# Performance work log

Hardware: AMD Instinct MI355X
Metric: run time of the kernel (lower is better)

Reference implementation:

```python
import jax, jax.numpy as jnp
import numpy as np

N = 100000   # nodes
E = 1600000  # edges (avg degree 16)
N_IN, N_HID, N_OUT = 64, 64, 16


def setup_inputs() -> dict:
    key = jax.random.key(0)
    k1, k2, k3, k4 = jax.random.split(key, 4)
    x = jax.random.normal(k1, (N, N_IN), dtype=jnp.float32)
    edge_index = jax.random.randint(k2, (2, E), 0, N, dtype=jnp.int64)
    # Glorot-style init like PyG GCNConv linear weights
    W1 = jax.random.normal(k3, (N_IN, N_HID), dtype=jnp.float32) * (1.0 / np.sqrt(N_IN))
    b1 = jnp.zeros((N_HID,), dtype=jnp.float32)
    W2 = jax.random.normal(k4, (N_HID, N_OUT), dtype=jnp.float32) * (1.0 / np.sqrt(N_HID))
    b2 = jnp.zeros((N_OUT,), dtype=jnp.float32)
    return {"x": x, "edge_index": edge_index, "W1": W1, "b1": b1, "W2": W2, "b2": b2}


def reference(x, edge_index, W1, b1, W2, b2):
    n = x.shape[0]
    # GCNConv default: add self-loops with weight 1, symmetric normalization
    loop = jnp.arange(n, dtype=edge_index.dtype)
    src = jnp.concatenate([edge_index[0], loop])  # [E+N]
    dst = jnp.concatenate([edge_index[1], loop])  # [E+N]
    w = jnp.ones(src.shape[0], dtype=x.dtype)
    deg = jax.ops.segment_sum(w, dst, num_segments=n)           # in-degree incl. self-loop
    dinv = jnp.where(deg > 0, jax.lax.rsqrt(deg), 0.0)
    norm = dinv[src] * w * dinv[dst]                            # [E+N] edge coefficients

    def gcn_conv(h, Wm, bm):
        h = h @ Wm                                              # [N, d_out] linear first (PyG order)
        msg = h[src] * norm[:, None]                            # gather + scale
        return jax.ops.segment_sum(msg, dst, num_segments=n) + bm  # scatter-add + bias

    h = jax.nn.relu(gcn_conv(x, W1, b1))
    # dropout is identity at inference (training=False)
    return jax.nn.log_softmax(gcn_conv(h, W2, b2), axis=1)
```

## Files before the change

kernel.cpp:

```cpp
#include <hip/hip_runtime.h>

constexpr int FIN = 64;
constexpr int FH  = 64;
constexpr int FO  = 16;


constexpr int BSH   = 7;
constexpr int BW    = 1 << BSH;
constexpr int NBUCK = 1024;
constexpr int EPB   = 16384;

constexpr int XT_STRIDE = 68;

__device__ inline unsigned short f2bf(float f) {
    unsigned u = __float_as_uint(f);
    return (unsigned short)((u + 0x7FFFu + ((u >> 16) & 1u)) >> 16);
}
__device__ inline float bf2f(unsigned short h) {
    return __uint_as_float((unsigned)h << 16);
}
__device__ inline float4 bf4_to_f4(ushort4 u) {
    float4 f;
    f.x = bf2f(u.x); f.y = bf2f(u.y); f.z = bf2f(u.z); f.w = bf2f(u.w);
    return f;
}

__launch_bounds__(256)
__global__ void gemm1_hist_kernel(const float* __restrict__ x, const float* __restrict__ W1,
                                  unsigned short* __restrict__ hsb,
                                  const int* __restrict__ ei, int E,
                                  int* __restrict__ bcnt, int N, int G1T) {
    __shared__ float smem[FIN * FH + 64 * XT_STRIDE];
    int tid = threadIdx.x;
    if ((int)blockIdx.x >= G1T) {
        int* lh = (int*)smem;
        for (int i = tid; i < NBUCK; i += 256) lh[i] = 0;
        __syncthreads();
        int base = ((int)blockIdx.x - G1T) * EPB;
        int lim  = min(E, base + EPB);
        for (int e = base + tid; e < lim; e += 256)
            atomicAdd(&lh[ei[E + e] >> BSH], 1);
        __syncthreads();
        for (int b = tid; b < NBUCK; b += 256) {
            int c = lh[b];
            if (c > 0) atomicAdd(&bcnt[b], c);
        }
        return;
    }
    float* Ws  = smem;
    float* xsT = smem + FIN * FH;
    {
        const float4* W14 = (const float4*)W1;
        float4* Ws4 = (float4*)Ws;
        for (int i = tid; i < 1024; i += 256) Ws4[i] = W14[i];
    }
    int rowBase = blockIdx.x * 64;
    const float4* x4 = (const float4*)x;
    #pragma unroll
    for (int p = 0; p < 4; ++p) {
        int f   = tid + p * 256;
        int row = f >> 4;
        int c4  = f & 15;
        int grow = rowBase + row;
        float4 v = (grow < N) ? x4[(size_t)grow * 16 + c4]
                              : make_float4(0.f, 0.f, 0.f, 0.f);
        xsT[(c4 * 4 + 0) * XT_STRIDE + row] = v.x;
        xsT[(c4 * 4 + 1) * XT_STRIDE + row] = v.y;
        xsT[(c4 * 4 + 2) * XT_STRIDE + row] = v.z;
        xsT[(c4 * 4 + 3) * XT_STRIDE + row] = v.w;
    }
    __syncthreads();
    int cg = tid & 15;
    int rg = tid >> 4;
    float4 a0 = {0,0,0,0}, a1 = {0,0,0,0}, a2 = {0,0,0,0}, a3 = {0,0,0,0};
    #pragma unroll 8
    for (int k = 0; k < FIN; ++k) {
        float4 wv = *(const float4*)&Ws[k * FH + cg * 4];
        float4 xv = *(const float4*)&xsT[k * XT_STRIDE + rg * 4];
        a0.x = fmaf(xv.x, wv.x, a0.x); a0.y = fmaf(xv.x, wv.y, a0.y);
        a0.z = fmaf(xv.x, wv.z, a0.z); a0.w = fmaf(xv.x, wv.w, a0.w);
        a1.x = fmaf(xv.y, wv.x, a1.x); a1.y = fmaf(xv.y, wv.y, a1.y);
        a1.z = fmaf(xv.y, wv.z, a1.z); a1.w = fmaf(xv.y, wv.w, a1.w);
        a2.x = fmaf(xv.z, wv.x, a2.x); a2.y = fmaf(xv.z, wv.y, a2.y);
        a2.z = fmaf(xv.z, wv.z, a2.z); a2.w = fmaf(xv.z, wv.w, a2.w);
        a3.x = fmaf(xv.w, wv.x, a3.x); a3.y = fmaf(xv.w, wv.y, a3.y);
        a3.z = fmaf(xv.w, wv.z, a3.z); a3.w = fmaf(xv.w, wv.w, a3.w);
    }
    ushort4* hsb4 = (ushort4*)hsb;
    {
        int grow = rowBase + rg * 4 + 0;
        if (grow < N) hsb4[(size_t)grow * 16 + cg] =
            make_ushort4(f2bf(a0.x), f2bf(a0.y), f2bf(a0.z), f2bf(a0.w));
        grow = rowBase + rg * 4 + 1;
        if (grow < N) hsb4[(size_t)grow * 16 + cg] =
            make_ushort4(f2bf(a1.x), f2bf(a1.y), f2bf(a1.z), f2bf(a1.w));
        grow = rowBase + rg * 4 + 2;
        if (grow < N) hsb4[(size_t)grow * 16 + cg] =
            make_ushort4(f2bf(a2.x), f2bf(a2.y), f2bf(a2.z), f2bf(a2.w));
        grow = rowBase + rg * 4 + 3;
        if (grow < N) hsb4[(size_t)grow * 16 + cg] =
            make_ushort4(f2bf(a3.x), f2bf(a3.y), f2bf(a3.z), f2bf(a3.w));
    }
}

__launch_bounds__(1024)
__global__ void bucket_scan_kernel(const int* __restrict__ bcnt, int* __restrict__ bbase,
                                   int* __restrict__ gcur, int* __restrict__ offs,
                                   int N, int E) {
    __shared__ int s[NBUCK];
    int t = threadIdx.x;
    int v = bcnt[t];
    s[t] = v;
    __syncthreads();
    for (int d = 1; d < NBUCK; d <<= 1) {
        int u = (t >= d) ? s[t - d] : 0;
        __syncthreads();
        s[t] += u;
        __syncthreads();
    }
    int ex = s[t] - v;
    bbase[t] = ex;
    gcur[t]  = ex;
    if (t == NBUCK - 1) {
        bbase[NBUCK] = s[t];
        offs[N] = E;
    }
}

__launch_bounds__(256)
__global__ void binning_kernel(const int* __restrict__ ei, int E,
                               int* __restrict__ gcur, unsigned* __restrict__ ebuf) {
    __shared__ int lh[NBUCK];
    int t = threadIdx.x;
    for (int i = t; i < NBUCK; i += 256) lh[i] = 0;
    __syncthreads();
    int base = blockIdx.x * EPB;
    int lim  = min(E, base + EPB);
    for (int e = base + t; e < lim; e += 256)
        atomicAdd(&lh[ei[E + e] >> BSH], 1);
    __syncthreads();
    for (int b = t; b < NBUCK; b += 256) {
        int c = lh[b];
        lh[b] = (c > 0) ? atomicAdd(&gcur[b], c) : 0;
    }
    __syncthreads();
    for (int e = base + t; e < lim; e += 256) {
        int d = ei[E + e];
        int srcv = ei[e];
        int pos = atomicAdd(&lh[d >> BSH], 1);
        ebuf[pos] = (unsigned)srcv | ((unsigned)(d & (BW - 1)) << 17);
    }
}

__launch_bounds__(256)
__global__ void bucket_csr_kernel(const unsigned* __restrict__ ebuf,
                                  const int* __restrict__ bbase,
                                  int* __restrict__ csr, int* __restrict__ offs,
                                  float* __restrict__ dinv, int N) {
    __shared__ int cnt[BW], sc[BW], cur[BW];
    int t = threadIdx.x;
    int b = blockIdx.x;
    if (t < BW) cnt[t] = 0;
    __syncthreads();
    int beg = bbase[b], end = bbase[b + 1];
    for (int i = beg + t; i < end; i += 256)
        atomicAdd(&cnt[ebuf[i] >> 17], 1);
    __syncthreads();
    if (t < BW) sc[t] = cnt[t];
    __syncthreads();
    for (int d = 1; d < BW; d <<= 1) {
        int u = (t < BW && t >= d) ? sc[t - d] : 0;
        __syncthreads();
        if (t < BW) sc[t] += u;
        __syncthreads();
    }
    int nodeBase = b << BSH;
    if (t < BW) {
        int node = nodeBase + t;
        int ex = beg + sc[t] - cnt[t];
        cur[t] = ex;
        if (node < N) {
            offs[node] = ex;
            dinv[node] = rsqrtf((float)(cnt[t] + 1));
        }
    }
    __syncthreads();
    for (int i = beg + t; i < end; i += 256) {
        unsigned w = ebuf[i];
        int pos = atomicAdd(&cur[w >> 17], 1);
        csr[pos] = (int)(w & 0x1FFFF);
    }
}

__launch_bounds__(256)
__global__ void agg1_gemm2_kernel(const unsigned short* __restrict__ hsb,
                                  const int* __restrict__ csr,
                                  const int* __restrict__ offs, const float* __restrict__ dinv,
                                  const float* __restrict__ b1, const float* __restrict__ W2,
                                  unsigned short* __restrict__ hs2b, int N) {
    __shared__ float W2s[FH * FO];
    __shared__ float h1s[16][68];
    const ushort4* hs4 = (const ushort4*)hsb;
    int tid = threadIdx.x;
    for (int i = tid; i < FH * FO; i += 256) W2s[i] = W2[i];
    int g = tid >> 4, l = tid & 15;
    int n = blockIdx.x * 16 + g;
    if (n < N) {
        float di_n = dinv[n];
        float4 self = bf4_to_f4(hs4[(size_t)n * 16 + l]);
        float4 acc;
        acc.x = self.x * di_n; acc.y = self.y * di_n;
        acc.z = self.z * di_n; acc.w = self.w * di_n;
        int j = offs[n], end = offs[n + 1];
        for (; j + 1 < end; j += 2) {
            int s0 = csr[j], s1 = csr[j + 1];
            float d0 = dinv[s0], d1 = dinv[s1];
            float4 a = bf4_to_f4(hs4[(size_t)s0 * 16 + l]);
            float4 b = bf4_to_f4(hs4[(size_t)s1 * 16 + l]);
            acc.x = fmaf(a.x, d0, fmaf(b.x, d1, acc.x));
            acc.y = fmaf(a.y, d0, fmaf(b.y, d1, acc.y));
            acc.z = fmaf(a.z, d0, fmaf(b.z, d1, acc.z));
            acc.w = fmaf(a.w, d0, fmaf(b.w, d1, acc.w));
        }
        if (j < end) {
            int s0 = csr[j];
            float d0 = dinv[s0];
            float4 a = bf4_to_f4(hs4[(size_t)s0 * 16 + l]);
            acc.x = fmaf(a.x, d0, acc.x); acc.y = fmaf(a.y, d0, acc.y);
            acc.z = fmaf(a.z, d0, acc.z); acc.w = fmaf(a.w, d0, acc.w);
        }
        float4 bb = ((const float4*)b1)[l];
        float4 h;
        h.x = fmaxf(fmaf(di_n, acc.x, bb.x), 0.f);
        h.y = fmaxf(fmaf(di_n, acc.y, bb.y), 0.f);
        h.z = fmaxf(fmaf(di_n, acc.z, bb.z), 0.f);
        h.w = fmaxf(fmaf(di_n, acc.w, bb.w), 0.f);
        *((float4*)&h1s[g][l * 4]) = h;
    }
    __syncthreads();
    int r = tid >> 4, o = tid & 15;
    int n2 = blockIdx.x * 16 + r;
    if (n2 < N) {
        float acc = 0.f;
        #pragma unroll
        for (int jj = 0; jj < FH; ++jj)
            acc = fmaf(h1s[r][jj], W2s[jj * FO + o], acc);
        hs2b[(size_t)n2 * FO + o] = f2bf(acc * dinv[n2]);
    }
}

__launch_bounds__(256)
__global__ void agg2_softmax_kernel(const unsigned short* __restrict__ hs2b,
                                    const int* __restrict__ csr,
                                    const int* __restrict__ offs, const float* __restrict__ dinv,
                                    const float* __restrict__ b2, float* __restrict__ out, int N) {
    int tid = threadIdx.x;
    int g = tid >> 4, o = tid & 15;
    int n = blockIdx.x * 16 + g;
    float v = 0.f;
    if (n < N) {
        float acc = bf2f(hs2b[(size_t)n * 16 + o]);
        int j = offs[n], end = offs[n + 1];
        for (; j + 1 < end; j += 2) {
            int s0 = csr[j], s1 = csr[j + 1];
            acc += bf2f(hs2b[(size_t)s0 * 16 + o]) + bf2f(hs2b[(size_t)s1 * 16 + o]);
        }
        if (j < end) acc += bf2f(hs2b[(size_t)csr[j] * 16 + o]);
        v = fmaf(dinv[n], acc, b2[o]);
    }
    float m = v;
    #pragma unroll
    for (int s = 8; s >= 1; s >>= 1) m = fmaxf(m, __shfl_xor(m, s, 64));
    float ex = __expf(v - m);
    float sum = ex;
    #pragma unroll
    for (int s = 8; s >= 1; s >>= 1) sum += __shfl_xor(sum, s, 64);
    if (n < N) out[(size_t)n * FO + o] = v - m - __logf(sum);
}

extern "C" void kernel_launch(void* const* d_in, const int* in_sizes, int n_in,
                              void* d_out, int out_size, void* d_ws, size_t ws_size,
                              hipStream_t stream) {
    const float* x  = (const float*)d_in[0];
    const int*   ei = (const int*)d_in[1];
    const float* W1 = (const float*)d_in[2];
    const float* b1 = (const float*)d_in[3];
    const float* W2 = (const float*)d_in[4];
    const float* b2 = (const float*)d_in[5];
    float* out = (float*)d_out;

    const int N = in_sizes[0] / FIN;
    const int E = in_sizes[1] / 2;
    const int NCHUNK = (E + EPB - 1) / EPB;
    const int NB4    = (N + BW - 1) / BW;
    const int G1T    = (N + 63) / 64;
    const int GA     = (N + 15) / 16;

    char* ws = (char*)d_ws;
    size_t off = 0;
    auto alloc = [&](size_t bytes) -> void* {
        off = (off + 255) & ~(size_t)255;
        void* p = ws + off;
        off += bytes;
        return p;
    };
    float*          dinv  = (float*)alloc((size_t)N * 4);
    unsigned short* hsb   = (unsigned short*)alloc((size_t)N * FH * 2);
    unsigned short* hs2b  = (unsigned short*)alloc((size_t)N * FO * 2);
    int*            offs  = (int*)alloc((size_t)(N + 1) * 4);
    int*            bcnt  = (int*)alloc(NBUCK * 4);
    int*            bbase = (int*)alloc((NBUCK + 1) * 4);
    int*            gcur  = (int*)alloc(NBUCK * 4);
    unsigned* ebuf;
    int*      csr;
    if (ws_size >= off + 512 + (size_t)E * 8) {
        ebuf = (unsigned*)alloc((size_t)E * 4);
        csr  = (int*)     alloc((size_t)E * 4);
    } else {
        ebuf = (unsigned*)x;
        csr  = (int*)x + E;
    }

    hipMemsetAsync(bcnt, 0, NBUCK * 4, stream);

    gemm1_hist_kernel<<<G1T + NCHUNK, 256, 0, stream>>>(x, W1, hsb, ei, E, bcnt, N, G1T);
    bucket_scan_kernel<<<1, NBUCK, 0, stream>>>(bcnt, bbase, gcur, offs, N, E);
    binning_kernel<<<NCHUNK, 256, 0, stream>>>(ei, E, gcur, ebuf);
    bucket_csr_kernel<<<NB4, 256, 0, stream>>>(ebuf, bbase, csr, offs, dinv, N);
    agg1_gemm2_kernel<<<GA, 256, 0, stream>>>(hsb, csr, offs, dinv, b1, W2, hs2b, N);
    agg2_softmax_kernel<<<GA, 256, 0, stream>>>(hs2b, csr, offs, dinv, b2, out, N);
}
```

Baseline: 242.3 us.

## Move GEMM1 to overlap with binning, shrink binning chunks, unroll gathers by four

The histogram now runs as its own small kernel, and the first GEMM is co-scheduled with the binning pass instead of the histogram pass. The heavier scatter work can then overlap the dense transform. Binning chunks shrink from 16384 to 4096 edges, giving more blocks and more parallelism for the scatter, at the cost of more global atomics on the bucket cursors. Both aggregation loops unroll from two to four neighbors to put more independent gathers in flight. When the workspace is too small, the aliased-x fallback keeps GEMM1 and binning as separate launches.

```diff
diff --git a/kernel.cpp b/kernel.cpp
--- a/kernel.cpp
+++ b/kernel.cpp
@@ -5,10 +5,11 @@
 constexpr int FO  = 16;
 
 
-constexpr int BSH   = 7;
-constexpr int BW    = 1 << BSH;
-constexpr int NBUCK = 1024;
-constexpr int EPB   = 16384;
+constexpr int BSH      = 7;
+constexpr int BW       = 1 << BSH;
+constexpr int NBUCK    = 1024;
+constexpr int EPB_HIST = 16384;
+constexpr int EPB_BIN  = 4096;
 
 constexpr int XT_STRIDE = 68;
 
@@ -26,25 +27,87 @@
 }
 
 __launch_bounds__(256)
-__global__ void gemm1_hist_kernel(const float* __restrict__ x, const float* __restrict__ W1,
-                                  unsigned short* __restrict__ hsb,
-                                  const int* __restrict__ ei, int E,
-                                  int* __restrict__ bcnt, int N, int G1T) {
+__global__ void hist_kernel(const int* __restrict__ ei, int E, int* __restrict__ bcnt) {
+    __shared__ int lh[NBUCK];
+    int t = threadIdx.x;
+    for (int i = t; i < NBUCK; i += 256) lh[i] = 0;
+    __syncthreads();
+    int base = blockIdx.x * EPB_HIST;
+    int lim  = min(E, base + EPB_HIST);
+    for (int e = base + t; e < lim; e += 256)
+        atomicAdd(&lh[ei[E + e] >> BSH], 1);
+    __syncthreads();
+    for (int b = t; b < NBUCK; b += 256) {
+        int c = lh[b];
+        if (c > 0) atomicAdd(&bcnt[b], c);
+    }
+}
+
+__launch_bounds__(1024)
+__global__ void bucket_scan_kernel(const int* __restrict__ bcnt, int* __restrict__ bbase,
+                                   int* __restrict__ gcur, int* __restrict__ offs,
+                                   int N, int E) {
+    __shared__ int s[NBUCK];
+    int t = threadIdx.x;
+    int v = bcnt[t];
+    s[t] = v;
+    __syncthreads();
+    for (int d = 1; d < NBUCK; d <<= 1) {
+        int u = (t >= d) ? s[t - d] : 0;
+        __syncthreads();
+        s[t] += u;
+        __syncthreads();
+    }
+    int ex = s[t] - v;
+    bbase[t] = ex;
+    gcur[t]  = ex;
+    if (t == NBUCK - 1) {
+        bbase[NBUCK] = s[t];
+        offs[N] = E;
+    }
+}
+
+__device__ inline void binning_body(const int* __restrict__ ei, int E, int chunk,
+                                    int* __restrict__ gcur, unsigned* __restrict__ ebuf,
+                                    int* lh) {
+    int t = threadIdx.x;
+    for (int i = t; i < NBUCK; i += 256) lh[i] = 0;
+    __syncthreads();
+    int base = chunk * EPB_BIN;
+    int lim  = min(E, base + EPB_BIN);
+    for (int e = base + t; e < lim; e += 256)
+        atomicAdd(&lh[ei[E + e] >> BSH], 1);
+    __syncthreads();
+    for (int b = t; b < NBUCK; b += 256) {
+        int c = lh[b];
+        lh[b] = (c > 0) ? atomicAdd(&gcur[b], c) : 0;
+    }
+    __syncthreads();
+    for (int e = base + t; e < lim; e += 256) {
+        int d = ei[E + e];
+        int srcv = ei[e];
+        int pos = atomicAdd(&lh[d >> BSH], 1);
+        ebuf[pos] = (unsigned)srcv | ((unsigned)(d & (BW - 1)) << 17);
+    }
+}
+
+__launch_bounds__(256)
+__global__ void binning_kernel(const int* __restrict__ ei, int E,
+                               int* __restrict__ gcur, unsigned* __restrict__ ebuf) {
+    __shared__ int lh[NBUCK];
+    binning_body(ei, E, blockIdx.x, gcur, ebuf, lh);
+}
+
+__launch_bounds__(256)
+__global__ void gemm1_binning_kernel(const float* __restrict__ x, const float* __restrict__ W1,
+                                     unsigned short* __restrict__ hsb,
+                                     const int* __restrict__ ei, int E,
+                                     int* __restrict__ gcur, unsigned* __restrict__ ebuf,
+                                     int N, int G1T) {
     __shared__ float smem[FIN * FH + 64 * XT_STRIDE];
     int tid = threadIdx.x;
     if ((int)blockIdx.x >= G1T) {
-        int* lh = (int*)smem;
-        for (int i = tid; i < NBUCK; i += 256) lh[i] = 0;
-        __syncthreads();
-        int base = ((int)blockIdx.x - G1T) * EPB;
-        int lim  = min(E, base + EPB);
-        for (int e = base + tid; e < lim; e += 256)
-            atomicAdd(&lh[ei[E + e] >> BSH], 1);
-        __syncthreads();
-        for (int b = tid; b < NBUCK; b += 256) {
-            int c = lh[b];
-            if (c > 0) atomicAdd(&bcnt[b], c);
-        }
+        binning_body(ei, E, (int)blockIdx.x - G1T, gcur, ebuf, (int*)smem);
         return;
     }
     float* Ws  = smem;
@@ -100,55 +163,6 @@
         grow = rowBase + rg * 4 + 3;
         if (grow < N) hsb4[(size_t)grow * 16 + cg] =
             make_ushort4(f2bf(a3.x), f2bf(a3.y), f2bf(a3.z), f2bf(a3.w));
-    }
-}
-
-__launch_bounds__(1024)
-__global__ void bucket_scan_kernel(const int* __restrict__ bcnt, int* __restrict__ bbase,
-                                   int* __restrict__ gcur, int* __restrict__ offs,
-                                   int N, int E) {
-    __shared__ int s[NBUCK];
-    int t = threadIdx.x;
-    int v = bcnt[t];
-    s[t] = v;
-    __syncthreads();
-    for (int d = 1; d < NBUCK; d <<= 1) {
-        int u = (t >= d) ? s[t - d] : 0;
-        __syncthreads();
-        s[t] += u;
-        __syncthreads();
-    }
-    int ex = s[t] - v;
-    bbase[t] = ex;
-    gcur[t]  = ex;
-    if (t == NBUCK - 1) {
-        bbase[NBUCK] = s[t];
-        offs[N] = E;
-    }
-}
-
-__launch_bounds__(256)
-__global__ void binning_kernel(const int* __restrict__ ei, int E,
-                               int* __restrict__ gcur, unsigned* __restrict__ ebuf) {
-    __shared__ int lh[NBUCK];
-    int t = threadIdx.x;
-    for (int i = t; i < NBUCK; i += 256) lh[i] = 0;
-    __syncthreads();
-    int base = blockIdx.x * EPB;
-    int lim  = min(E, base + EPB);
-    for (int e = base + t; e < lim; e += 256)
-        atomicAdd(&lh[ei[E + e] >> BSH], 1);
-    __syncthreads();
-    for (int b = t; b < NBUCK; b += 256) {
-        int c = lh[b];
-        lh[b] = (c > 0) ? atomicAdd(&gcur[b], c) : 0;
-    }
-    __syncthreads();
-    for (int e = base + t; e < lim; e += 256) {
-        int d = ei[E + e];
-        int srcv = ei[e];
-        int pos = atomicAdd(&lh[d >> BSH], 1);
-        ebuf[pos] = (unsigned)srcv | ((unsigned)(d & (BW - 1)) << 17);
     }
 }
 
@@ -212,17 +226,19 @@
         acc.x = self.x * di_n; acc.y = self.y * di_n;
         acc.z = self.z * di_n; acc.w = self.w * di_n;
         int j = offs[n], end = offs[n + 1];
-        for (; j + 1 < end; j += 2) {
-            int s0 = csr[j], s1 = csr[j + 1];
-            float d0 = dinv[s0], d1 = dinv[s1];
+        for (; j + 3 < end; j += 4) {
+            int s0 = csr[j], s1 = csr[j + 1], s2 = csr[j + 2], s3 = csr[j + 3];
+            float d0 = dinv[s0], d1 = dinv[s1], d2 = dinv[s2], d3 = dinv[s3];
             float4 a = bf4_to_f4(hs4[(size_t)s0 * 16 + l]);
             float4 b = bf4_to_f4(hs4[(size_t)s1 * 16 + l]);
-            acc.x = fmaf(a.x, d0, fmaf(b.x, d1, acc.x));
-            acc.y = fmaf(a.y, d0, fmaf(b.y, d1, acc.y));
-            acc.z = fmaf(a.z, d0, fmaf(b.z, d1, acc.z));
-            acc.w = fmaf(a.w, d0, fmaf(b.w, d1, acc.w));
+            float4 c = bf4_to_f4(hs4[(size_t)s2 * 16 + l]);
+            float4 d = bf4_to_f4(hs4[(size_t)s3 * 16 + l]);
+            acc.x = fmaf(a.x, d0, fmaf(b.x, d1, fmaf(c.x, d2, fmaf(d.x, d3, acc.x))));
+            acc.y = fmaf(a.y, d0, fmaf(b.y, d1, fmaf(c.y, d2, fmaf(d.y, d3, acc.y))));
+            acc.z = fmaf(a.z, d0, fmaf(b.z, d1, fmaf(c.z, d2, fmaf(d.z, d3, acc.z))));
+            acc.w = fmaf(a.w, d0, fmaf(b.w, d1, fmaf(c.w, d2, fmaf(d.w, d3, acc.w))));
         }
-        if (j < end) {
+        for (; j < end; ++j) {
             int s0 = csr[j];
             float d0 = dinv[s0];
             float4 a = bf4_to_f4(hs4[(size_t)s0 * 16 + l]);
@@ -261,11 +277,12 @@
     if (n < N) {
         float acc = bf2f(hs2b[(size_t)n * 16 + o]);
         int j = offs[n], end = offs[n + 1];
-        for (; j + 1 < end; j += 2) {
-            int s0 = csr[j], s1 = csr[j + 1];
-            acc += bf2f(hs2b[(size_t)s0 * 16 + o]) + bf2f(hs2b[(size_t)s1 * 16 + o]);
+        for (; j + 3 < end; j += 4) {
+            int s0 = csr[j], s1 = csr[j + 1], s2 = csr[j + 2], s3 = csr[j + 3];
+            acc += (bf2f(hs2b[(size_t)s0 * 16 + o]) + bf2f(hs2b[(size_t)s1 * 16 + o]))
+                 + (bf2f(hs2b[(size_t)s2 * 16 + o]) + bf2f(hs2b[(size_t)s3 * 16 + o]));
         }
-        if (j < end) acc += bf2f(hs2b[(size_t)csr[j] * 16 + o]);
+        for (; j < end; ++j) acc += bf2f(hs2b[(size_t)csr[j] * 16 + o]);
         v = fmaf(dinv[n], acc, b2[o]);
     }
     float m = v;
@@ -291,10 +308,11 @@
 
     const int N = in_sizes[0] / FIN;
     const int E = in_sizes[1] / 2;
-    const int NCHUNK = (E + EPB - 1) / EPB;
-    const int NB4    = (N + BW - 1) / BW;
-    const int G1T    = (N + 63) / 64;
-    const int GA     = (N + 15) / 16;
+    const int NCH  = (E + EPB_HIST - 1) / EPB_HIST;
+    const int NCB  = (E + EPB_BIN - 1) / EPB_BIN;
+    const int NB4  = (N + BW - 1) / BW;
+    const int G1T  = (N + 63) / 64;
+    const int GA   = (N + 15) / 16;
 
     char* ws = (char*)d_ws;
     size_t off = 0;
@@ -313,7 +331,8 @@
     int*            gcur  = (int*)alloc(NBUCK * 4);
     unsigned* ebuf;
     int*      csr;
-    if (ws_size >= off + 512 + (size_t)E * 8) {
+    bool ws_fits = (ws_size >= off + 512 + (size_t)E * 8);
+    if (ws_fits) {
         ebuf = (unsigned*)alloc((size_t)E * 4);
         csr  = (int*)     alloc((size_t)E * 4);
     } else {
@@ -323,9 +342,16 @@
 
     hipMemsetAsync(bcnt, 0, NBUCK * 4, stream);
 
-    gemm1_hist_kernel<<<G1T + NCHUNK, 256, 0, stream>>>(x, W1, hsb, ei, E, bcnt, N, G1T);
+    hist_kernel<<<NCH, 256, 0, stream>>>(ei, E, bcnt);
     bucket_scan_kernel<<<1, NBUCK, 0, stream>>>(bcnt, bbase, gcur, offs, N, E);
-    binning_kernel<<<NCHUNK, 256, 0, stream>>>(ei, E, gcur, ebuf);
+    if (ws_fits) {
+        gemm1_binning_kernel<<<G1T + NCB, 256, 0, stream>>>(x, W1, hsb, ei, E,
+                                                            gcur, ebuf, N, G1T);
+    } else {
+        gemm1_binning_kernel<<<G1T, 256, 0, stream>>>(x, W1, hsb, ei, E,
+                                                      gcur, ebuf, N, G1T);
+        binning_kernel<<<NCB, 256, 0, stream>>>(ei, E, gcur, ebuf);
+    }
     bucket_csr_kernel<<<NB4, 256, 0, stream>>>(ebuf, bbase, csr, offs, dinv, N);
     agg1_gemm2_kernel<<<GA, 256, 0, stream>>>(hsb, csr, offs, dinv, b1, W2, hs2b, N);
     agg2_softmax_kernel<<<GA, 256, 0, stream>>>(hs2b, csr, offs, dinv, b2, out, N);
```

After: 213.7 us. 11.8% less time.
